# Kernel tuning notes

Hardware: AMD Instinct MI355X
Metric: run time of the kernel (lower is better)

Reference implementation:

```python
import jax, jax.numpy as jnp
import numpy as np

B, S, D, H = 4, 2048, 1024, 1024  # batch, seq, input_dim, hidden_dim

def setup_inputs() -> dict:
    key = jax.random.key(0)
    k1, k2, k3, k4, k5 = jax.random.split(key, 5)
    scale1 = 1.0 / np.sqrt(D)
    scale2 = 1.0 / np.sqrt(H)
    return {
        "x": jax.random.normal(k1, (B, S, D), dtype=jnp.float32),
        "W1": jax.random.uniform(k2, (D, 3 * H), jnp.float32, -scale1, scale1),
        "b1": jax.random.uniform(k3, (3 * H,), jnp.float32, -scale1, scale1),
        "W2": jax.random.uniform(k4, (H, H), jnp.float32, -scale2, scale2),
        "b2": jax.random.uniform(k5, (H,), jnp.float32, -scale2, scale2),
    }

def reference(x, W1, b1, W2, b2):
    qkv = jnp.einsum('bsd,dh->bsh', x, W1) + b1          # [B,S,3H]
    q, k, v = jnp.split(qkv, 3, axis=-1)                  # each [B,S,H]
    scale = (2.0 * D) ** -0.5                             # faithful: (input_dim*2)^-0.5
    scores = jnp.einsum('bse,bSe->bsS', q, k) * scale     # [B,S,S]
    att = jax.nn.softmax(scores, axis=-1)
    ctx = jnp.einsum('bsS,bSe->bse', att, v)              # [B,S,H]
    out = jnp.einsum('bsh,hk->bsk', ctx, W2) + b2
    return out
```

## Files before the change

### kernel.cpp

```cpp
#include <hip/hip_runtime.h>
#include <hip/hip_bf16.h>
#include <stdint.h>

#define B_  4
#define S_  2048
#define D_  1024
#define H_  1024
#define BS_ (B_*S_)
#define N3H (3*H_)

typedef __bf16 bf16x8 __attribute__((ext_vector_type(8)));
typedef float  f32x4  __attribute__((ext_vector_type(4)));
typedef unsigned short u16x8 __attribute__((ext_vector_type(8)));

__device__ __forceinline__ unsigned short f2bf(float x) {
    unsigned u = __float_as_uint(x);
    return (unsigned short)((u + 0x7FFFu + ((u >> 16) & 1u)) >> 16);
}
__device__ __forceinline__ float bf2f(unsigned short h) {
    return __uint_as_float(((unsigned)h) << 16);
}

__device__ __forceinline__ void gload_lds16(const void* g, void* l) {
    __builtin_amdgcn_global_load_lds(
        (const __attribute__((address_space(1))) void*)g,
        (__attribute__((address_space(3))) void*)l, 16, 0, 0);
}

#define BAR __builtin_amdgcn_s_barrier()
#define DS_FENCE do { asm volatile("s_waitcnt lgkmcnt(0)" ::: "memory"); \
                      __builtin_amdgcn_sched_barrier(0); } while (0)

template<int EPI, int SWZ>
__global__ __launch_bounds__(256, 3) void gemm3b(
    const unsigned short* __restrict__ A,
    const unsigned short* __restrict__ Bm,
    int NXt, int NYt, int N, int K,
    long long sAz, long long sBz, long long sOz,
    void* __restrict__ out0, void* __restrict__ out1, void* __restrict__ out2,
    const float* __restrict__ bias, float scale)
{
    __shared__ __align__(16) char lds[3 * 16384];

    const int bid = (int)blockIdx.x;
    int tile;
    if constexpr (SWZ) {
        const int nt_g = (int)gridDim.x;
        const int C = nt_g >> 3;
        const int c = bid >> 3;
        const int xcd = bid & 7;
        const int qq = c >> 2;
        const int txl = qq % NXt;
        const int rest = (c & 3) + 4 * (qq / NXt);
        tile = xcd * C + rest * NXt + txl;
    } else {
        tile = bid;
    }
    const int tx = tile % NXt;
    const int rest2 = tile / NXt;
    const int ty = rest2 % NYt;
    const int tz = rest2 / NYt;

    const unsigned short* Ab = A  + (long long)tz * sAz;
    const unsigned short* Bb = Bm + (long long)tz * sBz;
    const int rowBase = ty * 128;
    const int colBase = tx * 128;
    const int tid = threadIdx.x;
    const int w = tid >> 6, l = tid & 63;
    const int wr = w >> 1, wc = w & 1;
    const int fr = l & 15, fq = l >> 4;

    int sr[2], scl[2];
#pragma unroll
    for (int j = 0; j < 2; j++) {
        int o  = j * 4096 + tid * 16;
        int st = o >> 10;
        int wi = o & 1023;
        wi ^= ((wi >> 9) & 1) << 5;
        sr[j]  = st * 16 + (wi >> 6);
        scl[j] = (wi & 63) >> 1;
    }

    auto STAGE_A = [&](char* buf, int t) {
        const unsigned short* base = Ab + (long long)rowBase * K + t * 32;
#pragma unroll
        for (int j = 0; j < 2; j++)
            gload_lds16(base + (long long)sr[j] * K + scl[j],
                        buf + j * 4096 + w * 1024);
    };
    auto STAGE_B = [&](char* buf, int t) {
        const unsigned short* base = Bb + (long long)colBase * K + t * 32;
#pragma unroll
        for (int j = 0; j < 2; j++)
            gload_lds16(base + (long long)sr[j] * K + scl[j],
                        buf + 8192 + j * 4096 + w * 1024);
    };

    const int abase = (fr * 64 + fq * 16) ^ ((fr & 8) << 2);

    f32x4 acc[4][4];
#pragma unroll
    for (int m = 0; m < 4; m++)
#pragma unroll
        for (int n = 0; n < 4; n++) acc[m][n] = (f32x4){0.f, 0.f, 0.f, 0.f};

    const int NT = K >> 5;

    STAGE_A(lds, 0); STAGE_B(lds, 0);
    STAGE_A(lds + 16384, 1); STAGE_B(lds + 16384, 1);
    asm volatile("s_waitcnt vmcnt(4)" ::: "memory");
    BAR;
    __builtin_amdgcn_sched_barrier(0);

    bf16x8 af[4], bf[4];

    for (int t = 0; t < NT; ++t) {
        const char* bc = lds + (t % 3) * 16384;
        char* bs = lds + ((t + 2) % 3) * 16384;
        int ts = t + 2; if (ts >= NT) ts -= NT;

#pragma unroll
        for (int m = 0; m < 4; m++)
            af[m] = *(const bf16x8*)(bc + (wr * 4 + m) * 1024 + abase);
#pragma unroll
        for (int n = 0; n < 4; n++)
            bf[n] = *(const bf16x8*)(bc + 8192 + (wc * 4 + n) * 1024 + abase);
        STAGE_A(bs, ts); STAGE_B(bs, ts);
        BAR; DS_FENCE;
        __builtin_amdgcn_s_setprio(1);
#pragma unroll
        for (int m = 0; m < 4; m++)
#pragma unroll
            for (int n = 0; n < 4; n++)
                acc[m][n] = __builtin_amdgcn_mfma_f32_16x16x32_bf16(
                    af[m], bf[n], acc[m][n], 0, 0, 0);
        __builtin_amdgcn_s_setprio(0);
        asm volatile("s_waitcnt vmcnt(4)" ::: "memory");
        BAR;
        __builtin_amdgcn_sched_barrier(0);
    }

    asm volatile("s_waitcnt vmcnt(0) lgkmcnt(0)" ::: "memory");
    BAR;

    const int crow0 = rowBase + wr * 64 + fq * 4;
    const int ccol0 = colBase + wc * 64 + fr;

    if constexpr (EPI == 0) {
        const int seg = colBase >> 10;
        if (seg < 2) {
            unsigned short* dst = (unsigned short*)(seg == 0 ? out0 : out1);
#pragma unroll
            for (int n = 0; n < 4; n++) {
                const int col = ccol0 + n * 16;
                const float bv = bias[col];
                const int scn = col & 1023;
#pragma unroll
                for (int m = 0; m < 4; m++) {
                    const int r0 = crow0 + m * 16;
#pragma unroll
                    for (int j = 0; j < 4; j++)
                        dst[(long long)(r0 + j) * 1024 + scn] = f2bf(acc[m][n][j] + bv);
                }
            }
        } else {
            unsigned short (*T)[129] = (unsigned short(*)[129])lds;
            const int lr0 = wr * 64 + fq * 4;
            const int lc0 = wc * 64 + fr;
#pragma unroll
            for (int n = 0; n < 4; n++) {
                const int lc = lc0 + n * 16;
#pragma unroll
                for (int m = 0; m < 4; m++)
#pragma unroll
                    for (int j = 0; j < 4; j++)
                        T[lr0 + m * 16 + j][lc] = f2bf(acc[m][n][j]);
            }
            BAR;
            const int s_loc = tid & 127, hh = tid >> 7;
            const int b = rowBase >> 11;
            const int s_glob = (rowBase & 2047) + s_loc;
            unsigned short* ut =
                (unsigned short*)out2 + (long long)b * ((long long)S_ * H_);
            const int h0 = (colBase - 2048) + hh * 64;
#pragma unroll 8
            for (int h = 0; h < 64; ++h)
                ut[(long long)(h0 + h) * S_ + s_glob] = T[s_loc][hh * 64 + h];
        }
    } else if constexpr (EPI == 1) {
        unsigned short* dst = (unsigned short*)out0 + (long long)tz * sOz;
#pragma unroll
        for (int n = 0; n < 4; n++) {
            const int col = ccol0 + n * 16;
#pragma unroll
            for (int m = 0; m < 4; m++) {
                const int r0 = crow0 + m * 16;
#pragma unroll
                for (int j = 0; j < 4; j++)
                    dst[(long long)(r0 + j) * N + col] = f2bf(acc[m][n][j] * scale);
            }
        }
    } else {
        float* dst = (float*)out0 + (long long)tz * sOz;
        const float* bu = (const float*)out1;
#pragma unroll
        for (int m = 0; m < 4; m++) {
            float linv[4];
#pragma unroll
            for (int j = 0; j < 4; j++)
                linv[j] = 1.0f / bias[tz * 2048 + crow0 + m * 16 + j];
#pragma unroll
            for (int n = 0; n < 4; n++) {
                const int col = ccol0 + n * 16;
                const float bvv = bu[col];
                const int r0 = crow0 + m * 16;
#pragma unroll
                for (int j = 0; j < 4; j++)
                    dst[(long long)(r0 + j) * N + col] = acc[m][n][j] * linv[j] + bvv;
            }
        }
        (void)scale;
    }
}

template<int EPI>
__global__ __launch_bounds__(512, 2) void gemm256(
    const unsigned short* __restrict__ A,
    const unsigned short* __restrict__ Bm,
    int NXt, int NYt, int N, int K,
    long long sAz, long long sBz, long long sOz,
    void* __restrict__ out0, void* __restrict__ out1, void* __restrict__ out2,
    const float* __restrict__ bias, float scale)
{
    __shared__ __align__(16) char lds[131072];

    const int nt_g = (int)gridDim.x;
    const int bid = (int)blockIdx.x;
    const int C = nt_g >> 3;
    const int c = bid >> 3;
    const int xcd = bid & 7;
    const int qq = c >> 2;
    const int txl = qq % NXt;
    const int rest = (c & 3) + 4 * (qq / NXt);
    const int tile = xcd * C + rest * NXt + txl;
    const int tx = tile % NXt;
    const int rest2 = tile / NXt;
    const int ty = rest2 % NYt;
    const int tz = rest2 / NYt;

    const unsigned short* Ab = A  + (long long)tz * sAz;
    const unsigned short* Bb = Bm + (long long)tz * sBz;
    const int rowBase = ty * 256;
    const int colBase = tx * 256;
    const int tid = threadIdx.x;
    const int w = tid >> 6, l = tid & 63;
    const int wr = w >> 2, wc = w & 3;
    const int fr = l & 15, fq = l >> 4;

    int sr[2], scl[2];
#pragma unroll
    for (int j = 0; j < 2; j++) {
        int o  = j * 8192 + tid * 16;
        int st = o >> 10;
        int wi = o & 1023;
        wi ^= ((wi >> 9) & 1) << 5;
        sr[j]  = (st >> 1) * 16 + (wi >> 6);
        scl[j] = (st & 1) * 32 + ((wi & 63) >> 1);
    }

    auto STAGE = [&](int buf, int which, int tile_) {
        const unsigned short* mat = (which < 2) ? Ab : Bb;
        const int rt0 = ((which < 2) ? rowBase : colBase) + (which & 1) * 128;
        char* dst = lds + buf * 65536 + (which >> 1) * 32768
                        + (which & 1) * 16384 + w * 1024;
        const int k0 = tile_ * 64;
#pragma unroll
        for (int j = 0; j < 2; j++) {
            const unsigned short* src =
                mat + (long long)(rt0 + sr[j]) * K + k0 + scl[j];
            gload_lds16(src, dst + j * 8192);
        }
    };

    const int abase = (fr * 64 + fq * 16) ^ ((fr & 8) << 2);
    const char* Ah[2] = { lds + wr * 16384, lds + 65536 + wr * 16384 };
    const char* Bh[2] = { lds + 32768 + (wc >> 1) * 16384,
                          lds + 98304 + (wc >> 1) * 16384 };
    const int bn0 = (wc & 1) * 8192;

#define LA(b, m, kk) (*(const bf16x8*)(Ah[b] + (m)*2048 + (kk)*1024 + abase))
#define LB(b, n, kk) (*(const bf16x8*)(Bh[b] + bn0 + (n)*2048 + (kk)*1024 + abase))
#define MFMA16(AF, BF, MOFF, NOFF) do { \
    __builtin_amdgcn_s_setprio(1); \
    _Pragma("unroll") for (int m_ = 0; m_ < 4; m_++) \
    _Pragma("unroll") for (int n_ = 0; n_ < 2; n_++) \
    _Pragma("unroll") for (int k_ = 0; k_ < 2; k_++) \
        acc[(MOFF)+m_][(NOFF)+n_] = __builtin_amdgcn_mfma_f32_16x16x32_bf16( \
            AF[m_][k_], BF[n_][k_], acc[(MOFF)+m_][(NOFF)+n_], 0, 0, 0); \
    __builtin_amdgcn_s_setprio(0); } while (0)

    f32x4 acc[8][4];
#pragma unroll
    for (int m = 0; m < 8; m++)
#pragma unroll
        for (int n = 0; n < 4; n++) acc[m][n] = (f32x4){0.f, 0.f, 0.f, 0.f};

    const int NT = K >> 6;

    STAGE(0, 0, 0); STAGE(0, 1, 0); STAGE(0, 2, 0); STAGE(0, 3, 0);
    STAGE(1, 0, 1); STAGE(1, 1, 1);
    asm volatile("s_waitcnt vmcnt(4)" ::: "memory");
    BAR;
    __builtin_amdgcn_sched_barrier(0);

    bf16x8 afA[4][2], afB[4][2], bfA[2][2], bfB[2][2];

    for (int i = 0; i < NT / 2; i++) {
        const int t1 = 2 * i + 1;
        int t2 = 2 * i + 2; if (t2 >= NT) t2 -= NT;
        int t3 = 2 * i + 3; if (t3 >= NT) t3 -= NT;

#pragma unroll
        for (int m = 0; m < 4; m++) { afA[m][0] = LA(0, m, 0); afA[m][1] = LA(0, m, 1); }
#pragma unroll
        for (int n = 0; n < 2; n++) { bfA[n][0] = LB(0, n, 0); bfA[n][1] = LB(0, n, 1); }
        STAGE(1, 2, t1);
        BAR; DS_FENCE;
        MFMA16(afA, bfA, 0, 0);
        BAR;
#pragma unroll
        for (int m = 0; m < 4; m++) { afB[m][0] = LA(0, 4 + m, 0); afB[m][1] = LA(0, 4 + m, 1); }
        STAGE(1, 3, t1);
        BAR; DS_FENCE;
        MFMA16(afB, bfA, 4, 0);
        BAR;
#pragma unroll
        for (int n = 0; n < 2; n++) { bfB[n][0] = LB(0, 2 + n, 0); bfB[n][1] = LB(0, 2 + n, 1); }
        STAGE(0, 0, t2);
        BAR; DS_FENCE;
        MFMA16(afA, bfB, 0, 2);
        BAR;
        STAGE(0, 1, t2);
        BAR;
        MFMA16(afB, bfB, 4, 2);
        asm volatile("s_waitcnt vmcnt(4)" ::: "memory");
        BAR;
        __builtin_amdgcn_sched_barrier(0);

#pragma unroll
        for (int m = 0; m < 4; m++) { afA[m][0] = LA(1, m, 0); afA[m][1] = LA(1, m, 1); }
#pragma unroll
        for (int n = 0; n < 2; n++) { bfA[n][0] = LB(1, n, 0); bfA[n][1] = LB(1, n, 1); }
        STAGE(0, 2, t2);
        BAR; DS_FENCE;
        MFMA16(afA, bfA, 0, 0);
        BAR;
#pragma unroll
        for (int m = 0; m < 4; m++) { afB[m][0] = LA(1, 4 + m, 0); afB[m][1] = LA(1, 4 + m, 1); }
        STAGE(0, 3, t2);
        BAR; DS_FENCE;
        MFMA16(afB, bfA, 4, 0);
        BAR;
#pragma unroll
        for (int n = 0; n < 2; n++) { bfB[n][0] = LB(1, 2 + n, 0); bfB[n][1] = LB(1, 2 + n, 1); }
        STAGE(1, 0, t3);
        BAR; DS_FENCE;
        MFMA16(afA, bfB, 0, 2);
        BAR;
        STAGE(1, 1, t3);
        BAR;
        MFMA16(afB, bfB, 4, 2);
        asm volatile("s_waitcnt vmcnt(4)" ::: "memory");
        BAR;
        __builtin_amdgcn_sched_barrier(0);
    }

    asm volatile("s_waitcnt vmcnt(0) lgkmcnt(0)" ::: "memory");

    const int crow0 = rowBase + wr * 128 + fq * 4;
    const int ccol0 = colBase + wc * 64 + fr;

    if constexpr (EPI == 2) {
        float* lsum = (float*)out1;
        unsigned short* dst = (unsigned short*)out0 + (long long)tz * sOz;
#pragma unroll
        for (int m = 0; m < 8; m++) {
#pragma unroll
            for (int j = 0; j < 4; j++) {
                const int row = crow0 + m * 16 + j;
                float rs = 0.f;
#pragma unroll
                for (int n = 0; n < 4; n++) {
                    const int col = ccol0 + n * 16;
                    const float p = __expf(acc[m][n][j] * scale);
                    const unsigned short us = f2bf(p);
                    dst[(long long)row * N + col] = us;
                    rs += bf2f(us);
                }
                rs += __shfl_xor(rs, 1); rs += __shfl_xor(rs, 2);
                rs += __shfl_xor(rs, 4); rs += __shfl_xor(rs, 8);
                if (fr == 0) atomicAdd(&lsum[tz * 2048 + row], rs);
            }
        }
    }
    (void)out2; (void)bias;
#undef LA
#undef LB
#undef MFMA16
}

__global__ __launch_bounds__(256) void conv_f32_bf16(
    const float* __restrict__ in, unsigned short* __restrict__ out, int n8)
{
    for (int i = blockIdx.x * blockDim.x + threadIdx.x; i < n8;
         i += gridDim.x * blockDim.x) {
        const float4 a = ((const float4*)in)[2 * i];
        const float4 b = ((const float4*)in)[2 * i + 1];
        u16x8 o;
        o[0] = f2bf(a.x); o[1] = f2bf(a.y); o[2] = f2bf(a.z); o[3] = f2bf(a.w);
        o[4] = f2bf(b.x); o[5] = f2bf(b.y); o[6] = f2bf(b.z); o[7] = f2bf(b.w);
        ((u16x8*)out)[i] = o;
    }
}

__global__ __launch_bounds__(256) void conv_w1v(
    const float* __restrict__ W1, unsigned short* __restrict__ w1v)
{
    const int i = blockIdx.x * 256 + threadIdx.x;
    const int j = i >> 7, hh = (i & 127) * 8;
    const float4 a = *(const float4*)&W1[(long long)j * 3072 + 2048 + hh];
    const float4 b = *(const float4*)&W1[(long long)j * 3072 + 2048 + hh + 4];
    u16x8 o;
    o[0] = f2bf(a.x); o[1] = f2bf(a.y); o[2] = f2bf(a.z); o[3] = f2bf(a.w);
    o[4] = f2bf(b.x); o[5] = f2bf(b.y); o[6] = f2bf(b.z); o[7] = f2bf(b.w);
    *(u16x8*)&w1v[(long long)j * 1024 + hh] = o;
}

__global__ __launch_bounds__(256) void bias_bu2(
    const float* __restrict__ b1, const unsigned short* __restrict__ w2t,
    const float* __restrict__ b2, float* __restrict__ bu2)
{
    const int i = blockIdx.x * 256 + threadIdx.x;
    float s = b2[i];
    for (int h8 = 0; h8 < 128; ++h8) {
        const u16x8 wv = *(const u16x8*)&w2t[(long long)i * 1024 + h8 * 8];
#pragma unroll
        for (int e = 0; e < 8; ++e)
            s += b1[2048 + h8 * 8 + e] * bf2f(wv[e]);
    }
    bu2[i] = s;
}

__global__ __launch_bounds__(256) void tconv_f32_bf16(
    const float* __restrict__ in, unsigned short* __restrict__ out,
    int rows, int cols)
{
    __shared__ float t[32][33];
    const int c0 = blockIdx.x * 32, r0 = blockIdx.y * 32;
    const int tx = threadIdx.x & 31, ty = threadIdx.x >> 5;
#pragma unroll
    for (int i = 0; i < 4; i++)
        t[ty + 8 * i][tx] = in[(long long)(r0 + ty + 8 * i) * cols + c0 + tx];
    __syncthreads();
#pragma unroll
    for (int i = 0; i < 4; i++)
        out[(long long)(c0 + ty + 8 * i) * rows + r0 + tx] = f2bf(t[tx][ty + 8 * i]);
}

extern "C" void kernel_launch(void* const* d_in, const int* in_sizes, int n_in,
                              void* d_out, int out_size, void* d_ws, size_t ws_size,
                              hipStream_t stream)
{
    (void)in_sizes; (void)n_in; (void)out_size; (void)ws_size;
    const float* x  = (const float*)d_in[0];
    const float* W1 = (const float*)d_in[1];
    const float* b1 = (const float*)d_in[2];
    const float* W2 = (const float*)d_in[3];
    const float* b2 = (const float*)d_in[4];
    float* out = (float*)d_out;

    char* ws = (char*)d_ws;
    size_t off = 0;
    auto alloc = [&](size_t bytes) {
        void* p = ws + off;
        off += (bytes + 255) & ~(size_t)255;
        return p;
    };
    unsigned short* xbf = (unsigned short*)alloc((size_t)BS_ * D_ * 2);
    unsigned short* w1t = (unsigned short*)alloc((size_t)N3H * D_ * 2);
    unsigned short* w2t = (unsigned short*)alloc((size_t)H_ * H_ * 2);
    unsigned short* w1v = (unsigned short*)alloc((size_t)D_ * H_ * 2);
    unsigned short* q   = (unsigned short*)alloc((size_t)BS_ * H_ * 2);
    unsigned short* k   = (unsigned short*)alloc((size_t)BS_ * H_ * 2);
    unsigned short* ut  = (unsigned short*)alloc((size_t)BS_ * H_ * 2);
    unsigned short* sc  = (unsigned short*)alloc((size_t)B_ * S_ * S_ * 2);
    float*          lsum = (float*)alloc((size_t)BS_ * 4);
    float*          bu2  = (float*)alloc((size_t)H_ * 4);

    const float scale = 0.022097086912079608f;

    hipMemsetAsync(lsum, 0, (size_t)BS_ * 4, stream);

    conv_f32_bf16<<<dim3(2048), dim3(256), 0, stream>>>(x, xbf, BS_ * D_ / 8);
    tconv_f32_bf16<<<dim3(N3H / 32, D_ / 32), dim3(256), 0, stream>>>(W1, w1t, D_, N3H);
    tconv_f32_bf16<<<dim3(H_ / 32, H_ / 32), dim3(256), 0, stream>>>(W2, w2t, H_, H_);
    conv_w1v<<<dim3(512), dim3(256), 0, stream>>>(W1, w1v);

    gemm3b<1, 0><<<dim3(64), dim3(256), 0, stream>>>(
        w2t, w1v, 8, 8, 1024, 1024, 0LL, 0LL, 0LL,
        w1t + (size_t)2048 * 1024, nullptr, nullptr, nullptr, 1.0f);

    bias_bu2<<<dim3(4), dim3(256), 0, stream>>>(b1, w2t, b2, bu2);

    gemm3b<0, 1><<<dim3(1536), dim3(256), 0, stream>>>(
        xbf, w1t, 24, 64, N3H, D_, 0LL, 0LL, 0LL, q, k, ut, b1, 1.0f);

    gemm256<2><<<dim3(256), dim3(512), 0, stream>>>(
        q, k, 8, 8, S_, H_, (long long)S_ * H_, (long long)S_ * H_,
        (long long)S_ * S_, sc, lsum, nullptr, nullptr, scale);

    gemm3b<5, 1><<<dim3(512), dim3(256), 0, stream>>>(
        sc, ut, 8, 16, H_, S_, (long long)S_ * S_, (long long)H_ * S_,
        (long long)S_ * H_, out, bu2, nullptr, lsum, 1.0f);
}
```

Baseline: 214.9 us.

## Split-K the weight-fusion GEMM and parallelize the bias reduction

The small W2ᵀ·W1v GEMM that runs as 64 blocks now uses split-K with 4 slices of K=256, giving 256 blocks. Each slice writes fp32 partials into the scratch score buffer, and a new reduce kernel sums them and converts the result to bf16. A row stride parameter is added to the GEMM so that the per-slice K can differ from the row stride. bias_bu2 now runs one block per output with a wave-shuffle reduction instead of 4 blocks each doing serial loops. The cost is an extra launch plus extra partial-sum traffic, all to remove a serial, under-occupied prologue.

```diff
diff --git a/kernel.cpp b/kernel.cpp
--- a/kernel.cpp
+++ b/kernel.cpp
@@ -12,6 +12,7 @@
 typedef __bf16 bf16x8 __attribute__((ext_vector_type(8)));
 typedef float  f32x4  __attribute__((ext_vector_type(4)));
 typedef unsigned short u16x8 __attribute__((ext_vector_type(8)));
+typedef unsigned short u16x4 __attribute__((ext_vector_type(4)));
 
 __device__ __forceinline__ unsigned short f2bf(float x) {
     unsigned u = __float_as_uint(x);
@@ -35,7 +36,7 @@
 __global__ __launch_bounds__(256, 3) void gemm3b(
     const unsigned short* __restrict__ A,
     const unsigned short* __restrict__ Bm,
-    int NXt, int NYt, int N, int K,
+    int NXt, int NYt, int N, int K, int Kst,
     long long sAz, long long sBz, long long sOz,
     void* __restrict__ out0, void* __restrict__ out1, void* __restrict__ out2,
     const float* __restrict__ bias, float scale)
@@ -82,17 +83,17 @@
     }
 
     auto STAGE_A = [&](char* buf, int t) {
-        const unsigned short* base = Ab + (long long)rowBase * K + t * 32;
+        const unsigned short* base = Ab + (long long)rowBase * Kst + t * 32;
 #pragma unroll
         for (int j = 0; j < 2; j++)
-            gload_lds16(base + (long long)sr[j] * K + scl[j],
+            gload_lds16(base + (long long)sr[j] * Kst + scl[j],
                         buf + j * 4096 + w * 1024);
     };
     auto STAGE_B = [&](char* buf, int t) {
-        const unsigned short* base = Bb + (long long)colBase * K + t * 32;
+        const unsigned short* base = Bb + (long long)colBase * Kst + t * 32;
 #pragma unroll
         for (int j = 0; j < 2; j++)
-            gload_lds16(base + (long long)sr[j] * K + scl[j],
+            gload_lds16(base + (long long)sr[j] * Kst + scl[j],
                         buf + 8192 + j * 4096 + w * 1024);
     };
 
@@ -187,8 +188,8 @@
             for (int h = 0; h < 64; ++h)
                 ut[(long long)(h0 + h) * S_ + s_glob] = T[s_loc][hh * 64 + h];
         }
-    } else if constexpr (EPI == 1) {
-        unsigned short* dst = (unsigned short*)out0 + (long long)tz * sOz;
+    } else if constexpr (EPI == 6) {
+        float* dst = (float*)out0 + (long long)tz * sOz;
 #pragma unroll
         for (int n = 0; n < 4; n++) {
             const int col = ccol0 + n * 16;
@@ -197,9 +198,10 @@
                 const int r0 = crow0 + m * 16;
 #pragma unroll
                 for (int j = 0; j < 4; j++)
-                    dst[(long long)(r0 + j) * N + col] = f2bf(acc[m][n][j] * scale);
+                    dst[(long long)(r0 + j) * N + col] = acc[m][n][j];
             }
         }
+        (void)scale; (void)bias;
     } else {
         float* dst = (float*)out0 + (long long)tz * sOz;
         const float* bu = (const float*)out1;
@@ -436,19 +438,36 @@
     *(u16x8*)&w1v[(long long)j * 1024 + hh] = o;
 }
 
+__global__ __launch_bounds__(256) void wu_reduce(
+    const float* __restrict__ part, unsigned short* __restrict__ dst)
+{
+    const int i = blockIdx.x * 256 + threadIdx.x;
+    f32x4 s = *(const f32x4*)&part[(long long)i * 4];
+#pragma unroll
+    for (int c = 1; c < 4; c++) {
+        const f32x4 p = *(const f32x4*)&part[(long long)c * 1048576 + (long long)i * 4];
+        s[0] += p[0]; s[1] += p[1]; s[2] += p[2]; s[3] += p[3];
+    }
+    u16x4 o;
+    o[0] = f2bf(s[0]); o[1] = f2bf(s[1]); o[2] = f2bf(s[2]); o[3] = f2bf(s[3]);
+    *(u16x4*)&dst[(long long)i * 4] = o;
+}
+
 __global__ __launch_bounds__(256) void bias_bu2(
     const float* __restrict__ b1, const unsigned short* __restrict__ w2t,
     const float* __restrict__ b2, float* __restrict__ bu2)
 {
-    const int i = blockIdx.x * 256 + threadIdx.x;
-    float s = b2[i];
-    for (int h8 = 0; h8 < 128; ++h8) {
-        const u16x8 wv = *(const u16x8*)&w2t[(long long)i * 1024 + h8 * 8];
-#pragma unroll
-        for (int e = 0; e < 8; ++e)
-            s += b1[2048 + h8 * 8 + e] * bf2f(wv[e]);
-    }
-    bu2[i] = s;
+    const int i = blockIdx.x;
+    const int t = threadIdx.x;
+    const u16x4 wv = *(const u16x4*)&w2t[(long long)i * 1024 + t * 4];
+    const float4 bv = *(const float4*)&b1[2048 + t * 4];
+    float s = bv.x * bf2f(wv[0]) + bv.y * bf2f(wv[1])
+            + bv.z * bf2f(wv[2]) + bv.w * bf2f(wv[3]);
+    for (int o = 32; o; o >>= 1) s += __shfl_xor(s, o);
+    __shared__ float red[4];
+    if ((t & 63) == 0) red[t >> 6] = s;
+    __syncthreads();
+    if (t == 0) bu2[i] = red[0] + red[1] + red[2] + red[3] + b2[i];
 }
 
 __global__ __launch_bounds__(256) void tconv_f32_bf16(
@@ -496,30 +515,32 @@
     unsigned short* sc  = (unsigned short*)alloc((size_t)B_ * S_ * S_ * 2);
     float*          lsum = (float*)alloc((size_t)BS_ * 4);
     float*          bu2  = (float*)alloc((size_t)H_ * 4);
+    float*          part = (float*)sc;
 
     const float scale = 0.022097086912079608f;
 
     hipMemsetAsync(lsum, 0, (size_t)BS_ * 4, stream);
 
     conv_f32_bf16<<<dim3(2048), dim3(256), 0, stream>>>(x, xbf, BS_ * D_ / 8);
-    tconv_f32_bf16<<<dim3(N3H / 32, D_ / 32), dim3(256), 0, stream>>>(W1, w1t, D_, N3H);
-    tconv_f32_bf16<<<dim3(H_ / 32, H_ / 32), dim3(256), 0, stream>>>(W2, w2t, H_, H_);
+    tconv_f32_bf16<<<dim3(64, 32), dim3(256), 0, stream>>>(W1, w1t, D_, N3H);
+    tconv_f32_bf16<<<dim3(32, 32), dim3(256), 0, stream>>>(W2, w2t, H_, H_);
     conv_w1v<<<dim3(512), dim3(256), 0, stream>>>(W1, w1v);
 
-    gemm3b<1, 0><<<dim3(64), dim3(256), 0, stream>>>(
-        w2t, w1v, 8, 8, 1024, 1024, 0LL, 0LL, 0LL,
-        w1t + (size_t)2048 * 1024, nullptr, nullptr, nullptr, 1.0f);
-
-    bias_bu2<<<dim3(4), dim3(256), 0, stream>>>(b1, w2t, b2, bu2);
+    gemm3b<6, 0><<<dim3(256), dim3(256), 0, stream>>>(
+        w2t, w1v, 8, 8, 1024, 256, 1024, 256LL, 256LL, (long long)H_ * H_,
+        part, nullptr, nullptr, nullptr, 1.0f);
+    wu_reduce<<<dim3(1024), dim3(256), 0, stream>>>(part, w1t + (size_t)2048 * 1024);
+
+    bias_bu2<<<dim3(1024), dim3(256), 0, stream>>>(b1, w2t, b2, bu2);
 
     gemm3b<0, 1><<<dim3(1536), dim3(256), 0, stream>>>(
-        xbf, w1t, 24, 64, N3H, D_, 0LL, 0LL, 0LL, q, k, ut, b1, 1.0f);
+        xbf, w1t, 24, 64, N3H, D_, D_, 0LL, 0LL, 0LL, q, k, ut, b1, 1.0f);
 
     gemm256<2><<<dim3(256), dim3(512), 0, stream>>>(
         q, k, 8, 8, S_, H_, (long long)S_ * H_, (long long)S_ * H_,
         (long long)S_ * S_, sc, lsum, nullptr, nullptr, scale);
 
     gemm3b<5, 1><<<dim3(512), dim3(256), 0, stream>>>(
-        sc, ut, 8, 16, H_, S_, (long long)S_ * S_, (long long)H_ * S_,
+        sc, ut, 8, 16, H_, S_, S_, (long long)S_ * S_, (long long)H_ * S_,
         (long long)S_ * H_, out, bu2, nullptr, lsum, 1.0f);
 }
```

New measurement: 190.0 us, median of 2. 11.5% less time.
